# Optimization experiments

Hardware: AMD Instinct MI355X
Metric: run time of the kernel (lower is better)

## Reference

```python
import jax, jax.numpy as jnp
import numpy as np

B, T, S = 32, 32, 400
H, E = 512, 300
V, MAX_OOV = 45000, 50
EXT_V = V + MAX_OOV
NEG = 1.0e12  # INF constant from the torch module


def setup_inputs() -> dict:
    key = jax.random.key(0)
    ks = jax.random.split(key, 16)
    p = lambda k, shape: jax.random.normal(k, shape, jnp.float32) * 0.02
    ext = jax.random.randint(ks[0], (B, S), 0, EXT_V, dtype=jnp.int64 if jax.config.jax_enable_x64 else jnp.int32)
    ext = ext.at[0, 0].set(EXT_V - 1)  # pin max OOV id so num_oov == MAX_OOV (matches torch data-dependent size)
    return {
        "trg_seq_embedded": jax.random.normal(ks[1], (B, T, E), jnp.float32),
        "ext_src_seq": ext,
        "init_states": jax.random.normal(ks[2], (1, B, H), jnp.float32),
        "encoder_outputs": jax.random.normal(ks[3], (B, S, H), jnp.float32),
        "encoder_mask": jnp.ones((B, S), jnp.int32),
        "W_enc": p(ks[4], (H, H)), "b_enc": jnp.zeros((H,), jnp.float32),
        "W_red": p(ks[5], (E, E + H)), "b_red": jnp.zeros((E,), jnp.float32),
        "W_ih": p(ks[6], (4 * H, E)), "W_hh": p(ks[7], (4 * H, H)),
        "b_ih": jnp.zeros((4 * H,), jnp.float32), "b_hh": jnp.zeros((4 * H,), jnp.float32),
        "W_cat": p(ks[8], (H, 2 * H)), "b_cat": jnp.zeros((H,), jnp.float32),
        "W_log": p(ks[9], (V, H)), "b_log": jnp.zeros((V,), jnp.float32),
    }


def reference(trg_seq_embedded, ext_src_seq, init_states, encoder_outputs, encoder_mask,
              W_enc, b_enc, W_red, b_red, W_ih, W_hh, b_ih, b_hh, W_cat, b_cat, W_log, b_log):
    batch = trg_seq_embedded.shape[0]
    # encoder features (memories): [B, S, H]
    memories = jnp.einsum('bsh,gh->bsg', encoder_outputs, W_enc) + b_enc
    batch_idx = jnp.arange(batch)[:, None]
    bias = b_ih + b_hh

    def step(carry, emb):
        h, c, ctx, cov = carry
        # reduce_layer on [embedded ; prev_context] -> [B, E]
        x = jnp.concatenate([emb, ctx], axis=-1) @ W_red.T + b_red
        # single-layer LSTM cell, torch gate order i,f,g,o
        gates = x @ W_ih.T + h @ W_hh.T + bias
        i_g, f_g, g_g, o_g = jnp.split(gates, 4, axis=-1)
        c_new = jax.nn.sigmoid(f_g) * c + jax.nn.sigmoid(i_g) * jnp.tanh(g_g)
        h_new = jax.nn.sigmoid(o_g) * jnp.tanh(c_new)
        # Bahdanau-style dot attention
        energy = jnp.einsum('bh,bsh->bs', h_new, memories)
        energy = jnp.where(encoder_mask == 0, -NEG, energy)
        attn = jax.nn.softmax(energy, axis=1)
        context = jnp.einsum('bs,bsh->bh', attn, memories)
        # output projection
        logit_in = jnp.tanh(jnp.concatenate([h_new, context], axis=-1) @ W_cat.T + b_cat)
        logit = logit_in @ W_log.T + b_log  # [B, V]
        # pointer: scatter_max of energies into extended vocabulary
        ext_logit = jnp.concatenate([logit, jnp.zeros((batch, EXT_V - V), logit.dtype)], axis=1)
        out = jnp.full((batch, EXT_V), -NEG, logit.dtype).at[batch_idx, ext_src_seq].max(energy)
        out = jnp.where(out == -NEG, 0.0, out)
        logit2 = ext_logit + out
        logit2 = jnp.where(logit2 == 0.0, -NEG, logit2)
        return (h_new, c_new, context, cov + attn), (logit2, attn, cov, energy)

    h0 = init_states[0]
    carry0 = (h0, h0, jnp.zeros((batch, memories.shape[-1]), trg_seq_embedded.dtype),
              jnp.zeros((batch, memories.shape[1]), trg_seq_embedded.dtype))
    _, (logits, attn_out, cov_out, energies) = jax.lax.scan(
        step, carry0, jnp.swapaxes(trg_seq_embedded, 0, 1))
    # each stacked over time: logits [T,B,EXT_V], attn/coverage/energies [T,B,S]
    return logits, attn_out, cov_out, energies
```

## Files before the change

### kernel.cpp

```cpp
#include <hip/hip_runtime.h>
#include <hip/hip_bf16.h>

typedef _Float16 h2 __attribute__((ext_vector_type(2)));
typedef _Float16 h8 __attribute__((ext_vector_type(8)));
typedef __attribute__((ext_vector_type(4))) float floatx4;
typedef __attribute__((ext_vector_type(2))) float f32x2;

#define NEGF 1.0e12f

#if __has_builtin(__builtin_amdgcn_fdot2)
#define DOT2(a,b,c) __builtin_amdgcn_fdot2((a),(b),(c),false)
#else
static __device__ __forceinline__ float DOT2(h2 a, h2 b, float c){
  return c + (float)a[0]*(float)b[0] + (float)a[1]*(float)b[1];
}
#endif

__device__ __forceinline__ float dot8(h8 a, h8 b, float c){
  h2 a0 = {a[0],a[1]}, a1 = {a[2],a[3]}, a2 = {a[4],a[5]}, a3 = {a[6],a[7]};
  h2 b0 = {b[0],b[1]}, b1 = {b[2],b[3]}, b2 = {b[4],b[5]}, b3 = {b[6],b[7]};
  c = DOT2(a0,b0,c); c = DOT2(a1,b1,c); c = DOT2(a2,b2,c); c = DOT2(a3,b3,c);
  return c;
}

__device__ __forceinline__ unsigned f16bits(float x){
  union { _Float16 h; unsigned short u; } cv; cv.h = (_Float16)x; return (unsigned)cv.u;
}

#define GLD_LDS16(g, l) __builtin_amdgcn_global_load_lds( \
    (const __attribute__((address_space(1))) void*)(g),   \
    (__attribute__((address_space(3))) void*)(l), 16, 0, 0)

#define ALOAD64(p)    __hip_atomic_load((p), __ATOMIC_RELAXED, __HIP_MEMORY_SCOPE_AGENT)
#define ALOAD32(p)    __hip_atomic_load((p), __ATOMIC_RELAXED, __HIP_MEMORY_SCOPE_AGENT)
#define ASTORE32(p,v) __hip_atomic_store((p), (v), __ATOMIC_RELAXED, __HIP_MEMORY_SCOPE_AGENT)

template<int EPI>
__global__ __launch_bounds__(256) void gemm_f16(
    const _Float16* __restrict__ A, const _Float16* __restrict__ B,
    float* __restrict__ Cf, _Float16* __restrict__ Ch,
    const float* __restrict__ bias, int N, int K, int ldc, int ntn)
{
  __shared__ char smem[32768];
  _Float16* Al = (_Float16*)smem;
  _Float16* Bl = (_Float16*)(smem + 16384);
  int bid = blockIdx.x;
  int bn, bm;
  if (EPI == 3) { bm = bid & 7; bn = bid >> 3; }
  else          { bn = bid % ntn; bm = bid / ntn; }
  int t = threadIdx.x;
  int w = t >> 6, l = t & 63;

  floatx4 acc[4][4];
#pragma unroll
  for (int i = 0; i < 4; ++i)
#pragma unroll
    for (int j = 0; j < 4; ++j) acc[i][j] = (floatx4){0.f, 0.f, 0.f, 0.f};

  const char* Ab = (const char*)A + (size_t)bm * 128 * K * 2;
  const char* Bb = (const char*)B + (size_t)bn * 128 * K * 2;
  const int rowb = K * 2;
  const int r0 = t >> 3;
  const int cbyte = ((t & 7) * 16) ^ (((t >> 3) & 7) << 4);
  char* AlB = (char*)Al;
  char* BlB = (char*)Bl;
  const int wm = (w >> 1) * 64, wn = (w & 1) * 64;

  for (int kt = 0; kt < K; kt += 64) {
    __syncthreads();
#pragma unroll
    for (int c = 0; c < 4; ++c) {
      int row = c * 32 + r0;
      GLD_LDS16(Ab + (size_t)row * rowb + kt * 2 + cbyte, AlB + c * 4096 + t * 16);
      GLD_LDS16(Bb + (size_t)row * rowb + kt * 2 + cbyte, BlB + c * 4096 + t * 16);
    }
    __syncthreads();
#pragma unroll
    for (int kk = 0; kk < 64; kk += 32) {
      h8 af[4], bfv[4];
#pragma unroll
      for (int i = 0; i < 4; ++i) {
        int ra = wm + i * 16 + (l & 15);
        int cb = ((kk << 1) + ((l >> 4) << 4)) ^ ((ra & 7) << 4);
        af[i] = *(const h8*)(AlB + ra * 128 + cb);
      }
#pragma unroll
      for (int j = 0; j < 4; ++j) {
        int ra = wn + j * 16 + (l & 15);
        int cb = ((kk << 1) + ((l >> 4) << 4)) ^ ((ra & 7) << 4);
        bfv[j] = *(const h8*)(BlB + ra * 128 + cb);
      }
#pragma unroll
      for (int i = 0; i < 4; ++i)
#pragma unroll
        for (int j = 0; j < 4; ++j)
          acc[i][j] = __builtin_amdgcn_mfma_f32_16x16x32_f16(af[i], bfv[j], acc[i][j], 0, 0, 0);
    }
  }

  if (EPI == 3) {
    float* Cs = (float*)smem;
#pragma unroll
    for (int half = 0; half < 2; ++half) {
      __syncthreads();
      if ((w >> 1) == half) {
        int rbase = ((l >> 4) << 2);
#pragma unroll
        for (int i = 0; i < 4; ++i)
#pragma unroll
          for (int j = 0; j < 4; ++j)
#pragma unroll
            for (int r = 0; r < 4; ++r)
              Cs[(i * 16 + rbase + r) * 128 + wn + j * 16 + (l & 15)] = acc[i][j][r];
      }
      __syncthreads();
#pragma unroll
      for (int rr = 0; rr < 16; ++rr) {
        int row = rr * 4 + w;
        int grow = bm * 128 + half * 64 + row;
        int cc = bn * 128 + 2 * l;
        float2 v = *(float2*)&Cs[row * 128 + 2 * l];
        float vv0, vv1;
        if (cc < N)     { float x0 = v.x + bias[cc];     vv0 = (x0 == 0.f) ? -NEGF : x0; } else vv0 = -NEGF;
        if (cc + 1 < N) { float x1 = v.y + bias[cc + 1]; vv1 = (x1 == 0.f) ? -NEGF : x1; } else vv1 = -NEGF;
        float* orow = Cf + (size_t)grow * ldc;
        if (cc + 1 < ldc) {
          f32x2 o; o.x = vv0; o.y = vv1;
          __builtin_nontemporal_store(o, (f32x2*)(orow + cc));
        } else if (cc < ldc) {
          __builtin_nontemporal_store(vv0, orow + cc);
        }
      }
    }
  } else {
    int mbase = bm * 128 + wm + ((l >> 4) << 2);
    int nbase = bn * 128 + wn + (l & 15);
#pragma unroll
    for (int j = 0; j < 4; ++j) {
      int col = nbase + j * 16;
#pragma unroll
      for (int i = 0; i < 4; ++i) {
#pragma unroll
        for (int r = 0; r < 4; ++r) {
          int row = mbase + i * 16 + r;
          float v = acc[i][j][r];
          if (col < N) {
            float bv = bias ? bias[col] : 0.f;
            if (EPI == 0)      Cf[(size_t)row * ldc + col] = v + bv;
            else if (EPI == 1) Ch[(size_t)row * ldc + col] = (_Float16)(v + bv);
            else               Ch[(size_t)row * ldc + col] = (_Float16)tanhf(v + bv);
          }
        }
      }
    }
  }
}

__device__ __forceinline__ void castseg(const float* __restrict__ src, _Float16* __restrict__ dst,
                                        int R, int C, int ld_src, int Cpad, int ld_dst, long i){
  int r = (int)(i / Cpad), c = (int)(i % Cpad);
  float v = (r < R && c < C) ? src[(size_t)r * ld_src + c] : 0.f;
  dst[(size_t)r * ld_dst + c] = (_Float16)v;
}

#define SB0 1280
#define SB1 26880
#define SB2 27904
#define SB3 28384
#define SB4 30944
#define SB5 32992
#define SB6 123104
#define SB7 127200
#define SB8 128480
#define SB9 129120

__global__ __launch_bounds__(256) void prep_kernel(
    const float* __restrict__ h0, const float* __restrict__ b_ih, const float* __restrict__ b_hh,
    const float* __restrict__ enc, const float* __restrict__ W_enc, const float* __restrict__ W_red,
    const float* __restrict__ W_ih, const float* __restrict__ W_cat, const float* __restrict__ W_log,
    const float* __restrict__ W_hh, const float* __restrict__ trg,
    _Float16* __restrict__ HCzT, float* __restrict__ bias_sum, _Float16* __restrict__ X1h,
    unsigned* __restrict__ bar, _Float16* __restrict__ enc_h, _Float16* __restrict__ W_enc_h,
    _Float16* __restrict__ Wr1_h, _Float16* __restrict__ W_ih_h, _Float16* __restrict__ W_cat_h,
    _Float16* __restrict__ W_log_h, _Float16* __restrict__ Wz, _Float16* __restrict__ emb_h,
    _Float16* __restrict__ Wr2T_h)
{
  int bid = blockIdx.x, t = threadIdx.x;
  if (bid < SB0) {
    long i = (long)bid * 256 + t;
    if (i < 32768) {
      int unit = (int)(i >> 3), pos = (int)(i & 7);
      int kc = unit >> 5, b = unit & 31;
      int k = kc * 8 + pos;
      HCzT[i] = (k < 512) ? (_Float16)h0[b * 512 + k] : (_Float16)0.f;
    }
    if (i < 2048)  bias_sum[i] = b_ih[i] + b_hh[i];
    if (i < 327680) X1h[i] = (_Float16)0.f;
    if (i < 1024) bar[i] = 0u;
  } else if (bid < SB1) {
    long i = (long)(bid - SB0) * 256 + t;
    castseg(enc, enc_h, 12800, 512, 512, 512, 512, i);
  } else if (bid < SB2) {
    long i = (long)(bid - SB1) * 256 + t;
    castseg(W_enc, W_enc_h, 512, 512, 512, 512, 512, i);
  } else if (bid < SB3) {
    long i = (long)(bid - SB2) * 256 + t;
    castseg(W_red, Wr1_h, 300, 300, 812, 320, 320, i);
  } else if (bid < SB4) {
    long i = (long)(bid - SB3) * 256 + t;
    castseg(W_ih, W_ih_h, 2048, 300, 300, 320, 320, i);
  } else if (bid < SB5) {
    long i = (long)(bid - SB4) * 256 + t;
    castseg(W_cat, W_cat_h, 512, 1024, 1024, 1024, 1024, i);
  } else if (bid < SB6) {
    long i = (long)(bid - SB5) * 256 + t;
    castseg(W_log, W_log_h, 45000, 512, 512, 512, 512, i);
  } else if (bid < SB7) {
    long i = (long)(bid - SB6) * 256 + t;
    castseg(W_hh, Wz, 2048, 512, 512, 512, 1024, i);
  } else if (bid < SB8) {
    int i = (bid - SB7) * 256 + t;
    int m = i / 320, e = i % 320;
    int tt = m >> 5, b = m & 31;
    float v = (e < 300) ? trg[((size_t)b * 32 + tt) * 300 + e] : 0.f;
    emb_h[i] = (_Float16)v;
  } else if (bid < SB9) {
    int i = (bid - SB8) * 256 + t;
    int h = i / 320, e = i % 320;
    float v = (e < 300) ? W_red[(size_t)e * 812 + 300 + h] : 0.f;
    Wr2T_h[i] = (_Float16)v;
  }
}

__device__ __forceinline__ void gbar(unsigned* flags, unsigned gen){
  asm volatile("s_waitcnt vmcnt(0)" ::: "memory");
  __syncthreads();
  if (threadIdx.x == 0) {
    ASTORE32(flags + blockIdx.x, gen);
    for (;;) {
      bool done = true;
#pragma unroll
      for (int i = 0; i < 32; ++i)
        done &= (ALOAD32(flags + i) >= gen);
      if (done) break;
      __builtin_amdgcn_s_sleep(2);
    }
  }
  __syncthreads();
  asm volatile("" ::: "memory");
}

__global__ __launch_bounds__(512, 1) void fused_loop(
    const _Float16* __restrict__ memh, _Float16* __restrict__ HCzT,
    _Float16* __restrict__ HC_A, const _Float16* __restrict__ Wz,
    const float* __restrict__ P, const float* __restrict__ inits,
    const int* __restrict__ mask, float* __restrict__ e_out,
    float* __restrict__ a_out, float* __restrict__ c_out, unsigned* __restrict__ bar)
{
  __shared__ char smem[32768];
  __shared__ __align__(16) float es[400];
  __shared__ float red[16];
  __shared__ float cum[400];
  __shared__ _Float16 hh[512];

  float* gl = (float*)smem;
  const int q = blockIdx.x, t = threadIdx.x;
  const int w = t >> 6, l = t & 63;
  const int mw = w >> 2, nw = w & 3;

  if (t < 400) cum[t] = 0.f;

  float creg = inits[(t >> 4) * 512 + q * 16 + (t & 15)];
  const _Float16* mb = memh + (size_t)q * 400 * 512;

  const _Float16* wbase[4];
#pragma unroll
  for (int s = 0; s < 4; ++s)
    wbase[s] = Wz + (size_t)(s * 512 + q * 16 + (l & 15)) * 1024 + nw * 256 + ((l >> 4) << 3);

  __syncthreads();

  for (int ts = 0; ts < 32; ++ts) {
    {
      unsigned long long* zsrc = (unsigned long long*)(HCzT + (size_t)ts * 32768);
      floatx4 acc[4];
#pragma unroll
      for (int s = 0; s < 4; ++s) acc[s] = (floatx4){0.f, 0.f, 0.f, 0.f};
#pragma unroll
      for (int kk8 = 0; kk8 < 8; ++kk8) {
        int unit = ((nw * 8 + kk8) * 4 + (l >> 4)) * 32 + mw * 16 + (l & 15);
        union { unsigned long long u[2]; h8 v; } za;
        za.u[0] = ALOAD64(zsrc + (size_t)unit * 2);
        za.u[1] = ALOAD64(zsrc + (size_t)unit * 2 + 1);
#pragma unroll
        for (int s = 0; s < 4; ++s) {
          h8 wv = *(const h8*)(wbase[s] + kk8 * 32);
          acc[s] = __builtin_amdgcn_mfma_f32_16x16x32_f16(za.v, wv, acc[s], 0, 0, 0);
        }
      }
#pragma unroll
      for (int s = 0; s < 4; ++s)
#pragma unroll
        for (int r = 0; r < 4; ++r) {
          int b = mw * 16 + ((l >> 4) << 2) + r;
          gl[(s * 4 + nw) * 512 + b * 16 + (l & 15)] = acc[s][r];
        }
    }
    __syncthreads();
    {
      int b = t >> 4, j16 = t & 15;
      const float* Pr = P + ((size_t)ts * 32 + b) * 2048 + q * 16 + j16;
      float g4[4];
#pragma unroll
      for (int s = 0; s < 4; ++s)
        g4[s] = gl[(s * 4 + 0) * 512 + t] + gl[(s * 4 + 1) * 512 + t]
              + gl[(s * 4 + 2) * 512 + t] + gl[(s * 4 + 3) * 512 + t] + Pr[s * 512];
      float ig = 1.f / (1.f + expf(-g4[0]));
      float fg = 1.f / (1.f + expf(-g4[1]));
      float og = 1.f / (1.f + expf(-g4[3]));
      float cn = fg * creg + ig * tanhf(g4[2]);
      float hn = og * tanhf(cn);
      creg = cn;
      unsigned hu = f16bits(hn);
      unsigned other = __shfl_xor(hu, 1);
      if (!(t & 1)) {
        unsigned pack = hu | (other << 16);
        int j = q * 16 + j16;
        unsigned* dst = (unsigned*)((char*)(HCzT + (size_t)(ts + 1) * 32768)
                                    + (((j >> 3) * 32 + b) << 4) + ((j & 7) << 1));
        ASTORE32(dst, pack);
        *(unsigned*)(HC_A + ((size_t)ts * 32 + b) * 1024 + j) = pack;
      }
    }
    gbar(bar, 2 * ts + 1);

    size_t obase = (size_t)ts * 12800 + q * 400;
    {
      if (t < 64) {
        unsigned long long* hsrc = (unsigned long long*)(HCzT + (size_t)(ts + 1) * 32768);
        union { unsigned long long u[2]; h8 v; } ha;
        ha.u[0] = ALOAD64(hsrc + ((size_t)t * 32 + q) * 2);
        ha.u[1] = ALOAD64(hsrc + ((size_t)t * 32 + q) * 2 + 1);
        *(h8*)&hh[t * 8] = ha.v;
      }
      __syncthreads();

      {
        int g = l >> 2, c = l & 3;
#pragma unroll
        for (int r = 0; r < 4; ++r) {
          int sr = r * 16 + g;
          if (sr < 50) {
            int s = w * 50 + sr;
            const _Float16* row = mb + (size_t)s * 512 + c * 128;
            float e = 0.f;
#pragma unroll
            for (int k = 0; k < 16; ++k)
              e = dot8(*(const h8*)(row + k * 8), *(const h8*)&hh[c * 128 + k * 8], e);
            e += __shfl_xor(e, 1);
            e += __shfl_xor(e, 2);
            if (c == 0) {
              if (mask[q * 400 + s] == 0) e = -NEGF;
              es[s] = e;
            }
          }
        }
      }
      __syncthreads();
      if (t < 400) e_out[obase + t] = es[t];

      float v = (t < 400) ? es[t] : -3.4e38f;
      float m = v;
#pragma unroll
      for (int o = 32; o; o >>= 1) m = fmaxf(m, __shfl_xor(m, o));
      if (l == 0) red[w] = m;
      __syncthreads();
      m = red[0];
#pragma unroll
      for (int qq = 1; qq < 8; ++qq) m = fmaxf(m, red[qq]);
      float p = (t < 400) ? expf(v - m) : 0.f;
      float sum = p;
#pragma unroll
      for (int o = 32; o; o >>= 1) sum += __shfl_xor(sum, o);
      if (l == 0) red[8 + w] = sum;
      __syncthreads();
      float tot = red[8];
#pragma unroll
      for (int qq = 9; qq < 16; ++qq) tot += red[qq];
      float inv = 1.f / tot;
      float aval = p * inv;
      if (t < 400) {
        es[t] = aval;
        a_out[obase + t] = aval;
        c_out[obase + t] = cum[t];
        cum[t] += aval;
      }
      __syncthreads();

      float a0 = 0.f, a1 = 0.f, a2 = 0.f, a3 = 0.f;
#pragma unroll 4
      for (int si = 0; si < 400; si += 4) {
        a0 += es[si + 0] * (float)mb[(size_t)(si + 0) * 512 + t];
        a1 += es[si + 1] * (float)mb[(size_t)(si + 1) * 512 + t];
        a2 += es[si + 2] * (float)mb[(size_t)(si + 2) * 512 + t];
        a3 += es[si + 3] * (float)mb[(size_t)(si + 3) * 512 + t];
      }
      float acc2 = (a0 + a1) + (a2 + a3);
      unsigned cu = f16bits(acc2);
      unsigned other = __shfl_xor(cu, 1);
      if (!(t & 1)) {
        unsigned pack = cu | (other << 16);
        int kg = 512 + t;
        unsigned* dst = (unsigned*)((char*)(HCzT + (size_t)(ts + 1) * 32768)
                                    + (((kg >> 3) * 32 + q) << 4) + ((kg & 7) << 1));
        ASTORE32(dst, pack);
        *(unsigned*)(HC_A + ((size_t)ts * 32 + q) * 1024 + kg) = pack;
      }
    }
    gbar(bar, 2 * ts + 2);
  }
}

__global__ __launch_bounds__(512) void pointer_kernel(
    const int* __restrict__ ext, const float* __restrict__ energ, float* __restrict__ logits)
{
  __shared__ int ids[400];
  __shared__ float es[400];
  int tb = blockIdx.x;
  int b = tb & 31;
  int tt = tb >> 5;
  int t = threadIdx.x;
  if (t < 400) {
    ids[t] = ext[b * 400 + t];
    es[t] = energ[(size_t)tt * 12800 + b * 400 + t];
  }
  __syncthreads();
  if (t < 400) {
    int id = ids[t];
    bool first = true;
    for (int s = 0; s < t; ++s) if (ids[s] == id) { first = false; break; }
    if (first) {
      float mx = es[t];
      for (int s = t + 1; s < 400; ++s) if (ids[s] == id) mx = fmaxf(mx, es[s]);
      if (mx != -NEGF) {
        float* p = &logits[(size_t)tb * 45050 + id];
        float base = 0.f;
        if (id < 45000) { float cur = *p; base = (cur == -NEGF) ? 0.f : cur; }
        float nv = base + mx;
        *p = (nv == 0.f) ? -NEGF : nv;
      }
    }
  }
}

extern "C" void kernel_launch(void* const* d_in, const int* in_sizes, int n_in,
                              void* d_out, int out_size, void* d_ws, size_t ws_size,
                              hipStream_t stream) {
  const float* trg   = (const float*)d_in[0];
  const int*   ext   = (const int*)d_in[1];
  const float* inits = (const float*)d_in[2];
  const float* enc   = (const float*)d_in[3];
  const int*   mask  = (const int*)d_in[4];
  const float* W_enc = (const float*)d_in[5];
  const float* b_enc = (const float*)d_in[6];
  const float* W_red = (const float*)d_in[7];
  const float* b_red = (const float*)d_in[8];
  const float* W_ih  = (const float*)d_in[9];
  const float* W_hh  = (const float*)d_in[10];
  const float* b_ih  = (const float*)d_in[11];
  const float* b_hh  = (const float*)d_in[12];
  const float* W_cat = (const float*)d_in[13];
  const float* b_cat = (const float*)d_in[14];
  const float* W_log = (const float*)d_in[15];
  const float* b_log = (const float*)d_in[16];

  float* out = (float*)d_out;
  float* out_logits = out;
  float* out_attn   = out + 46131200;
  float* out_cov    = out_attn + 409600;
  float* out_energy = out_cov + 409600;

  char* ws = (char*)d_ws;
  size_t o = 0;
  auto alloc = [&](size_t bytes) { void* p = ws + o; o += (bytes + 255) & ~(size_t)255; return p; };
  _Float16* mem_h   = (_Float16*)alloc(12800ULL * 512 * 2);
  _Float16* enc_h   = (_Float16*)alloc(12800ULL * 512 * 2);
  _Float16* W_enc_h = (_Float16*)alloc(512ULL * 512 * 2);
  _Float16* emb_h   = (_Float16*)alloc(1024ULL * 320 * 2);
  _Float16* Wr1_h   = (_Float16*)alloc(384ULL * 320 * 2);
  _Float16* X1_h    = (_Float16*)alloc(1024ULL * 320 * 2);
  _Float16* W_ih_h  = (_Float16*)alloc(2048ULL * 320 * 2);
  _Float16* Wr2T_h  = (_Float16*)alloc(512ULL * 320 * 2);
  _Float16* W_cat_h = (_Float16*)alloc(512ULL * 1024 * 2);
  _Float16* W_log_h = (_Float16*)alloc(45056ULL * 512 * 2);
  _Float16* A_log_h = (_Float16*)alloc(1024ULL * 512 * 2);
  _Float16* HCzT    = (_Float16*)alloc(33ULL * 32768 * 2);
  _Float16* HC_A    = (_Float16*)alloc(1024ULL * 1024 * 2);
  _Float16* Wz      = (_Float16*)alloc(2048ULL * 1024 * 2);
  float* P        = (float*)alloc(1024ULL * 2048 * 4);
  float* bias_sum = (float*)alloc(2048ULL * 4);
  unsigned* bar   = (unsigned*)alloc(4096);

  prep_kernel<<<SB9, 256, 0, stream>>>(
      inits, b_ih, b_hh, enc, W_enc, W_red, W_ih, W_cat, W_log, W_hh, trg,
      HCzT, bias_sum, X1_h, bar, enc_h, W_enc_h, Wr1_h, W_ih_h, W_cat_h,
      W_log_h, Wz, emb_h, Wr2T_h);

  gemm_f16<1><<<400, 256, 0, stream>>>(enc_h, W_enc_h, nullptr, mem_h, b_enc, 512, 512, 512, 4);
  gemm_f16<1><<<24,  256, 0, stream>>>(emb_h, Wr1_h, nullptr, X1_h, b_red, 300, 320, 320, 3);
  gemm_f16<0><<<128, 256, 0, stream>>>(X1_h, W_ih_h, P, nullptr, bias_sum, 2048, 320, 2048, 16);
  gemm_f16<1><<<64,  256, 0, stream>>>(W_ih_h, Wr2T_h, nullptr, Wz + 512, nullptr, 512, 320, 1024, 4);

  fused_loop<<<32, 512, 0, stream>>>(mem_h, HCzT, HC_A, Wz, P, inits, mask,
                                     out_energy, out_attn, out_cov, bar);

  gemm_f16<2><<<32, 256, 0, stream>>>(HC_A, W_cat_h, nullptr, A_log_h, b_cat, 512, 1024, 512, 4);
  gemm_f16<3><<<2816, 256, 0, stream>>>(A_log_h, W_log_h, out_logits, nullptr, b_log, 45000, 512, 45050, 352);
  pointer_kernel<<<1024, 512, 0, stream>>>(ext, out_energy, out_logits);
}
```

Before: 1.186 ms.

## Overlap vocab projection GEMMs with the recurrent loop inside one persistent kernel

Merges the recurrent loop, the W_cat projection and the vocabulary logits GEMM into a single persistent kernel of 256 blocks. The first 32 blocks run the timestep recurrence and publish a progress counter. The other 224 blocks wait on that counter, then compute the tanh(W_cat) and W_log GEMMs for each completed chunk of 4 timesteps while later steps are still running. The aim is to hide the large logits GEMM behind the latency-bound recurrence. In exchange it adds spin-wait synchronisation, assumes all 256 blocks are co-resident, and drops the separate GEMM launches.

```diff
diff --git a/kernel.cpp b/kernel.cpp
--- a/kernel.cpp
+++ b/kernel.cpp
@@ -45,9 +45,7 @@
   _Float16* Al = (_Float16*)smem;
   _Float16* Bl = (_Float16*)(smem + 16384);
   int bid = blockIdx.x;
-  int bn, bm;
-  if (EPI == 3) { bm = bid & 7; bn = bid >> 3; }
-  else          { bn = bid % ntn; bm = bid / ntn; }
+  int bn = bid % ntn, bm = bid / ntn;
   int t = threadIdx.x;
   int w = t >> 6, l = t & 63;
 
@@ -98,58 +96,126 @@
     }
   }
 
-  if (EPI == 3) {
-    float* Cs = (float*)smem;
-#pragma unroll
-    for (int half = 0; half < 2; ++half) {
-      __syncthreads();
-      if ((w >> 1) == half) {
-        int rbase = ((l >> 4) << 2);
+  int mbase = bm * 128 + wm + ((l >> 4) << 2);
+  int nbase = bn * 128 + wn + (l & 15);
+#pragma unroll
+  for (int j = 0; j < 4; ++j) {
+    int col = nbase + j * 16;
+#pragma unroll
+    for (int i = 0; i < 4; ++i) {
+#pragma unroll
+      for (int r = 0; r < 4; ++r) {
+        int row = mbase + i * 16 + r;
+        float v = acc[i][j][r];
+        if (col < N) {
+          float bv = bias ? bias[col] : 0.f;
+          if (EPI == 0) Cf[(size_t)row * ldc + col] = v + bv;
+          else          Ch[(size_t)row * ldc + col] = (_Float16)(v + bv);
+        }
+      }
+    }
+  }
+}
+
+template<int EPI>
+__device__ void wgemm(const _Float16* __restrict__ Aext, int lda,
+                      const _Float16* __restrict__ B,
+                      float* __restrict__ Cf, _Float16* __restrict__ Alog,
+                      const float* __restrict__ bias,
+                      int N, int K, int ldc, int bm, int bn, char* smem)
+{
+  int t = threadIdx.x;
+  bool act = t < 256;
+  int w = t >> 6, l = t & 63;
+  floatx4 acc[4][4];
+#pragma unroll
+  for (int i = 0; i < 4; ++i)
+#pragma unroll
+    for (int j = 0; j < 4; ++j) acc[i][j] = (floatx4){0.f, 0.f, 0.f, 0.f};
+
+  const char* Bb = (const char*)B + (size_t)bn * 128 * K * 2;
+  const int rowb = K * 2;
+  const int r0 = t >> 3;
+  const int cbyte = ((t & 7) * 16) ^ (((t >> 3) & 7) << 4);
+  char* BlB = smem;
+  const int wm = (w >> 1) * 64, wn = (w & 1) * 64;
+
+  for (int kt = 0; kt < K; kt += 64) {
+    __syncthreads();
+    if (act) {
+#pragma unroll
+      for (int c = 0; c < 4; ++c) {
+        int row = c * 32 + r0;
+        GLD_LDS16(Bb + (size_t)row * rowb + kt * 2 + cbyte, BlB + c * 4096 + t * 16);
+      }
+    }
+    __syncthreads();
+    if (act) {
+#pragma unroll
+      for (int kk = 0; kk < 64; kk += 32) {
+        h8 af[4], bfv[4];
+#pragma unroll
+        for (int i = 0; i < 4; ++i) {
+          int ra = wm + i * 16 + (l & 15);
+          unsigned long long* ap = (unsigned long long*)
+              (Aext + (size_t)ra * lda + kt + kk + ((l >> 4) << 3));
+          union { unsigned long long u[2]; h8 v; } ua;
+          ua.u[0] = ALOAD64(ap); ua.u[1] = ALOAD64(ap + 1);
+          af[i] = ua.v;
+        }
+#pragma unroll
+        for (int j = 0; j < 4; ++j) {
+          int ra = wn + j * 16 + (l & 15);
+          int cb = ((kk << 1) + ((l >> 4) << 4)) ^ ((ra & 7) << 4);
+          bfv[j] = *(const h8*)(BlB + ra * 128 + cb);
+        }
 #pragma unroll
         for (int i = 0; i < 4; ++i)
 #pragma unroll
           for (int j = 0; j < 4; ++j)
-#pragma unroll
-            for (int r = 0; r < 4; ++r)
-              Cs[(i * 16 + rbase + r) * 128 + wn + j * 16 + (l & 15)] = acc[i][j][r];
-      }
-      __syncthreads();
+            acc[i][j] = __builtin_amdgcn_mfma_f32_16x16x32_f16(af[i], bfv[j], acc[i][j], 0, 0, 0);
+      }
+    }
+  }
+
+  float* Cs = (float*)smem;
+#pragma unroll
+  for (int half = 0; half < 2; ++half) {
+    __syncthreads();
+    if (act && (w >> 1) == half) {
+      int rbase = ((l >> 4) << 2);
+#pragma unroll
+      for (int i = 0; i < 4; ++i)
+#pragma unroll
+        for (int j = 0; j < 4; ++j)
+#pragma unroll
+          for (int r = 0; r < 4; ++r)
+            Cs[(i * 16 + rbase + r) * 128 + wn + j * 16 + (l & 15)] = acc[i][j][r];
+    }
+    __syncthreads();
+    if (act) {
 #pragma unroll
       for (int rr = 0; rr < 16; ++rr) {
         int row = rr * 4 + w;
         int grow = bm * 128 + half * 64 + row;
         int cc = bn * 128 + 2 * l;
         float2 v = *(float2*)&Cs[row * 128 + 2 * l];
-        float vv0, vv1;
-        if (cc < N)     { float x0 = v.x + bias[cc];     vv0 = (x0 == 0.f) ? -NEGF : x0; } else vv0 = -NEGF;
-        if (cc + 1 < N) { float x1 = v.y + bias[cc + 1]; vv1 = (x1 == 0.f) ? -NEGF : x1; } else vv1 = -NEGF;
-        float* orow = Cf + (size_t)grow * ldc;
-        if (cc + 1 < ldc) {
-          f32x2 o; o.x = vv0; o.y = vv1;
-          __builtin_nontemporal_store(o, (f32x2*)(orow + cc));
-        } else if (cc < ldc) {
-          __builtin_nontemporal_store(vv0, orow + cc);
-        }
-      }
-    }
-  } else {
-    int mbase = bm * 128 + wm + ((l >> 4) << 2);
-    int nbase = bn * 128 + wn + (l & 15);
-#pragma unroll
-    for (int j = 0; j < 4; ++j) {
-      int col = nbase + j * 16;
-#pragma unroll
-      for (int i = 0; i < 4; ++i) {
-#pragma unroll
-        for (int r = 0; r < 4; ++r) {
-          int row = mbase + i * 16 + r;
-          float v = acc[i][j][r];
-          if (col < N) {
-            float bv = bias ? bias[col] : 0.f;
-            if (EPI == 0)      Cf[(size_t)row * ldc + col] = v + bv;
-            else if (EPI == 1) Ch[(size_t)row * ldc + col] = (_Float16)(v + bv);
-            else               Ch[(size_t)row * ldc + col] = (_Float16)tanhf(v + bv);
+        if (EPI == 3) {
+          float vv0, vv1;
+          if (cc < N)     { float x0 = v.x + bias[cc];     vv0 = (x0 == 0.f) ? -NEGF : x0; } else vv0 = -NEGF;
+          if (cc + 1 < N) { float x1 = v.y + bias[cc + 1]; vv1 = (x1 == 0.f) ? -NEGF : x1; } else vv1 = -NEGF;
+          float* orow = Cf + (size_t)grow * ldc;
+          if (cc + 1 < ldc) {
+            f32x2 o; o.x = vv0; o.y = vv1;
+            __builtin_nontemporal_store(o, (f32x2*)(orow + cc));
+          } else if (cc < ldc) {
+            __builtin_nontemporal_store(vv0, orow + cc);
           }
+        } else {
+          float x0 = tanhf(v.x + bias[cc]);
+          float x1 = tanhf(v.y + bias[cc + 1]);
+          unsigned pack = f16bits(x0) | (f16bits(x1) << 16);
+          ASTORE32((unsigned*)(Alog + (size_t)grow * 512 + cc), pack);
         }
       }
     }
@@ -250,12 +316,15 @@
   asm volatile("" ::: "memory");
 }
 
-__global__ __launch_bounds__(512, 1) void fused_loop(
+__global__ __launch_bounds__(512, 1) void fused_all(
     const _Float16* __restrict__ memh, _Float16* __restrict__ HCzT,
     _Float16* __restrict__ HC_A, const _Float16* __restrict__ Wz,
     const float* __restrict__ P, const float* __restrict__ inits,
     const int* __restrict__ mask, float* __restrict__ e_out,
-    float* __restrict__ a_out, float* __restrict__ c_out, unsigned* __restrict__ bar)
+    float* __restrict__ a_out, float* __restrict__ c_out, unsigned* __restrict__ bar,
+    const _Float16* __restrict__ W_cat_h, const float* __restrict__ b_cat,
+    _Float16* __restrict__ A_log, const _Float16* __restrict__ W_log_h,
+    const float* __restrict__ b_log, float* __restrict__ logits)
 {
   __shared__ char smem[32768];
   __shared__ __align__(16) float es[400];
@@ -263,161 +332,193 @@
   __shared__ float cum[400];
   __shared__ _Float16 hh[512];
 
-  float* gl = (float*)smem;
-  const int q = blockIdx.x, t = threadIdx.x;
-  const int w = t >> 6, l = t & 63;
-  const int mw = w >> 2, nw = w & 3;
-
-  if (t < 400) cum[t] = 0.f;
-
-  float creg = inits[(t >> 4) * 512 + q * 16 + (t & 15)];
-  const _Float16* mb = memh + (size_t)q * 400 * 512;
-
-  const _Float16* wbase[4];
-#pragma unroll
-  for (int s = 0; s < 4; ++s)
-    wbase[s] = Wz + (size_t)(s * 512 + q * 16 + (l & 15)) * 1024 + nw * 256 + ((l >> 4) << 3);
-
-  __syncthreads();
-
-  for (int ts = 0; ts < 32; ++ts) {
-    {
-      unsigned long long* zsrc = (unsigned long long*)(HCzT + (size_t)ts * 32768);
-      floatx4 acc[4];
-#pragma unroll
-      for (int s = 0; s < 4; ++s) acc[s] = (floatx4){0.f, 0.f, 0.f, 0.f};
-#pragma unroll
-      for (int kk8 = 0; kk8 < 8; ++kk8) {
-        int unit = ((nw * 8 + kk8) * 4 + (l >> 4)) * 32 + mw * 16 + (l & 15);
-        union { unsigned long long u[2]; h8 v; } za;
-        za.u[0] = ALOAD64(zsrc + (size_t)unit * 2);
-        za.u[1] = ALOAD64(zsrc + (size_t)unit * 2 + 1);
-#pragma unroll
-        for (int s = 0; s < 4; ++s) {
-          h8 wv = *(const h8*)(wbase[s] + kk8 * 32);
-          acc[s] = __builtin_amdgcn_mfma_f32_16x16x32_f16(za.v, wv, acc[s], 0, 0, 0);
-        }
-      }
-#pragma unroll
-      for (int s = 0; s < 4; ++s)
-#pragma unroll
-        for (int r = 0; r < 4; ++r) {
-          int b = mw * 16 + ((l >> 4) << 2) + r;
-          gl[(s * 4 + nw) * 512 + b * 16 + (l & 15)] = acc[s][r];
-        }
-    }
+  const int blk = blockIdx.x, t = threadIdx.x;
+
+  if (blk < 32) {
+    float* gl = (float*)smem;
+    const int q = blk;
+    const int w = t >> 6, l = t & 63;
+    const int mw = w >> 2, nw = w & 3;
+
+    if (t < 400) cum[t] = 0.f;
+
+    float creg = inits[(t >> 4) * 512 + q * 16 + (t & 15)];
+    const _Float16* mb = memh + (size_t)q * 400 * 512;
+
+    const _Float16* wbase[4];
+#pragma unroll
+    for (int s = 0; s < 4; ++s)
+      wbase[s] = Wz + (size_t)(s * 512 + q * 16 + (l & 15)) * 1024 + nw * 256 + ((l >> 4) << 3);
+
     __syncthreads();
-    {
-      int b = t >> 4, j16 = t & 15;
-      const float* Pr = P + ((size_t)ts * 32 + b) * 2048 + q * 16 + j16;
-      float g4[4];
-#pragma unroll
-      for (int s = 0; s < 4; ++s)
-        g4[s] = gl[(s * 4 + 0) * 512 + t] + gl[(s * 4 + 1) * 512 + t]
-              + gl[(s * 4 + 2) * 512 + t] + gl[(s * 4 + 3) * 512 + t] + Pr[s * 512];
-      float ig = 1.f / (1.f + expf(-g4[0]));
-      float fg = 1.f / (1.f + expf(-g4[1]));
-      float og = 1.f / (1.f + expf(-g4[3]));
-      float cn = fg * creg + ig * tanhf(g4[2]);
-      float hn = og * tanhf(cn);
-      creg = cn;
-      unsigned hu = f16bits(hn);
-      unsigned other = __shfl_xor(hu, 1);
-      if (!(t & 1)) {
-        unsigned pack = hu | (other << 16);
-        int j = q * 16 + j16;
-        unsigned* dst = (unsigned*)((char*)(HCzT + (size_t)(ts + 1) * 32768)
-                                    + (((j >> 3) * 32 + b) << 4) + ((j & 7) << 1));
-        ASTORE32(dst, pack);
-        *(unsigned*)(HC_A + ((size_t)ts * 32 + b) * 1024 + j) = pack;
-      }
-    }
-    gbar(bar, 2 * ts + 1);
-
-    size_t obase = (size_t)ts * 12800 + q * 400;
-    {
-      if (t < 64) {
-        unsigned long long* hsrc = (unsigned long long*)(HCzT + (size_t)(ts + 1) * 32768);
-        union { unsigned long long u[2]; h8 v; } ha;
-        ha.u[0] = ALOAD64(hsrc + ((size_t)t * 32 + q) * 2);
-        ha.u[1] = ALOAD64(hsrc + ((size_t)t * 32 + q) * 2 + 1);
-        *(h8*)&hh[t * 8] = ha.v;
+
+    for (int ts = 0; ts < 32; ++ts) {
+      {
+        unsigned long long* zsrc = (unsigned long long*)(HCzT + (size_t)ts * 32768);
+        floatx4 acc[4];
+#pragma unroll
+        for (int s = 0; s < 4; ++s) acc[s] = (floatx4){0.f, 0.f, 0.f, 0.f};
+#pragma unroll
+        for (int kk8 = 0; kk8 < 8; ++kk8) {
+          int unit = ((nw * 8 + kk8) * 4 + (l >> 4)) * 32 + mw * 16 + (l & 15);
+          union { unsigned long long u[2]; h8 v; } za;
+          za.u[0] = ALOAD64(zsrc + (size_t)unit * 2);
+          za.u[1] = ALOAD64(zsrc + (size_t)unit * 2 + 1);
+#pragma unroll
+          for (int s = 0; s < 4; ++s) {
+            h8 wv = *(const h8*)(wbase[s] + kk8 * 32);
+            acc[s] = __builtin_amdgcn_mfma_f32_16x16x32_f16(za.v, wv, acc[s], 0, 0, 0);
+          }
+        }
+#pragma unroll
+        for (int s = 0; s < 4; ++s)
+#pragma unroll
+          for (int r = 0; r < 4; ++r) {
+            int b = mw * 16 + ((l >> 4) << 2) + r;
+            gl[(s * 4 + nw) * 512 + b * 16 + (l & 15)] = acc[s][r];
+          }
       }
       __syncthreads();
-
       {
-        int g = l >> 2, c = l & 3;
-#pragma unroll
-        for (int r = 0; r < 4; ++r) {
-          int sr = r * 16 + g;
-          if (sr < 50) {
-            int s = w * 50 + sr;
-            const _Float16* row = mb + (size_t)s * 512 + c * 128;
-            float e = 0.f;
-#pragma unroll
-            for (int k = 0; k < 16; ++k)
-              e = dot8(*(const h8*)(row + k * 8), *(const h8*)&hh[c * 128 + k * 8], e);
-            e += __shfl_xor(e, 1);
-            e += __shfl_xor(e, 2);
-            if (c == 0) {
-              if (mask[q * 400 + s] == 0) e = -NEGF;
-              es[s] = e;
+        int b = t >> 4, j16 = t & 15;
+        const float* Pr = P + ((size_t)ts * 32 + b) * 2048 + q * 16 + j16;
+        float g4[4];
+#pragma unroll
+        for (int s = 0; s < 4; ++s)
+          g4[s] = gl[(s * 4 + 0) * 512 + t] + gl[(s * 4 + 1) * 512 + t]
+                + gl[(s * 4 + 2) * 512 + t] + gl[(s * 4 + 3) * 512 + t] + Pr[s * 512];
+        float ig = 1.f / (1.f + expf(-g4[0]));
+        float fg = 1.f / (1.f + expf(-g4[1]));
+        float og = 1.f / (1.f + expf(-g4[3]));
+        float cn = fg * creg + ig * tanhf(g4[2]);
+        float hn = og * tanhf(cn);
+        creg = cn;
+        unsigned hu = f16bits(hn);
+        unsigned other = __shfl_xor(hu, 1);
+        if (!(t & 1)) {
+          unsigned pack = hu | (other << 16);
+          int j = q * 16 + j16;
+          unsigned* dst = (unsigned*)((char*)(HCzT + (size_t)(ts + 1) * 32768)
+                                      + (((j >> 3) * 32 + b) << 4) + ((j & 7) << 1));
+          ASTORE32(dst, pack);
+          ASTORE32((unsigned*)(HC_A + ((size_t)ts * 32 + b) * 1024 + j), pack);
+        }
+      }
+      gbar(bar, 2 * ts + 1);
+
+      size_t obase = (size_t)ts * 12800 + q * 400;
+      {
+        if (t < 64) {
+          unsigned long long* hsrc = (unsigned long long*)(HCzT + (size_t)(ts + 1) * 32768);
+          union { unsigned long long u[2]; h8 v; } ha;
+          ha.u[0] = ALOAD64(hsrc + ((size_t)t * 32 + q) * 2);
+          ha.u[1] = ALOAD64(hsrc + ((size_t)t * 32 + q) * 2 + 1);
+          *(h8*)&hh[t * 8] = ha.v;
+        }
+        __syncthreads();
+
+        {
+          int g = l >> 2, c = l & 3;
+#pragma unroll
+          for (int r = 0; r < 4; ++r) {
+            int sr = r * 16 + g;
+            if (sr < 50) {
+              int s = w * 50 + sr;
+              const _Float16* row = mb + (size_t)s * 512 + c * 128;
+              float e = 0.f;
+#pragma unroll
+              for (int k = 0; k < 16; ++k)
+                e = dot8(*(const h8*)(row + k * 8), *(const h8*)&hh[c * 128 + k * 8], e);
+              e += __shfl_xor(e, 1);
+              e += __shfl_xor(e, 2);
+              if (c == 0) {
+                if (mask[q * 400 + s] == 0) e = -NEGF;
+                es[s] = e;
+              }
             }
           }
         }
+        __syncthreads();
+        if (t < 400) e_out[obase + t] = es[t];
+
+        float v = (t < 400) ? es[t] : -3.4e38f;
+        float m = v;
+#pragma unroll
+        for (int o = 32; o; o >>= 1) m = fmaxf(m, __shfl_xor(m, o));
+        if (l == 0) red[w] = m;
+        __syncthreads();
+        m = red[0];
+#pragma unroll
+        for (int qq = 1; qq < 8; ++qq) m = fmaxf(m, red[qq]);
+        float p = (t < 400) ? expf(v - m) : 0.f;
+        float sum = p;
+#pragma unroll
+        for (int o = 32; o; o >>= 1) sum += __shfl_xor(sum, o);
+        if (l == 0) red[8 + w] = sum;
+        __syncthreads();
+        float tot = red[8];
+#pragma unroll
+        for (int qq = 9; qq < 16; ++qq) tot += red[qq];
+        float inv = 1.f / tot;
+        float aval = p * inv;
+        if (t < 400) {
+          es[t] = aval;
+          a_out[obase + t] = aval;
+          c_out[obase + t] = cum[t];
+          cum[t] += aval;
+        }
+        __syncthreads();
+
+        float a0 = 0.f, a1 = 0.f, a2 = 0.f, a3 = 0.f;
+#pragma unroll 4
+        for (int si = 0; si < 400; si += 4) {
+          a0 += es[si + 0] * (float)mb[(size_t)(si + 0) * 512 + t];
+          a1 += es[si + 1] * (float)mb[(size_t)(si + 1) * 512 + t];
+          a2 += es[si + 2] * (float)mb[(size_t)(si + 2) * 512 + t];
+          a3 += es[si + 3] * (float)mb[(size_t)(si + 3) * 512 + t];
+        }
+        float acc2 = (a0 + a1) + (a2 + a3);
+        unsigned cu = f16bits(acc2);
+        unsigned other = __shfl_xor(cu, 1);
+        if (!(t & 1)) {
+          unsigned pack = cu | (other << 16);
+          int kg = 512 + t;
+          unsigned* dst = (unsigned*)((char*)(HCzT + (size_t)(ts + 1) * 32768)
+                                      + (((kg >> 3) * 32 + q) << 4) + ((kg & 7) << 1));
+          ASTORE32(dst, pack);
+          ASTORE32((unsigned*)(HC_A + ((size_t)ts * 32 + q) * 1024 + kg), pack);
+        }
+      }
+      gbar(bar, 2 * ts + 2);
+      if (blk == 0 && t == 0) ASTORE32(bar + 256, (unsigned)(ts + 1));
+    }
+  } else {
+    int wid = blk - 32;
+    unsigned* prog = bar + 256;
+    unsigned* cnt  = bar + 512;
+    for (int c = 0; c < 8; ++c) {
+      if (t == 0) {
+        while (ALOAD32(prog) < (unsigned)(4 * c + 4)) __builtin_amdgcn_s_sleep(8);
       }
       __syncthreads();
-      if (t < 400) e_out[obase + t] = es[t];
-
-      float v = (t < 400) ? es[t] : -3.4e38f;
-      float m = v;
-#pragma unroll
-      for (int o = 32; o; o >>= 1) m = fmaxf(m, __shfl_xor(m, o));
-      if (l == 0) red[w] = m;
+      if (wid >= c * 4 && wid < c * 4 + 4) {
+        wgemm<2>(HC_A + (size_t)c * 128 * 1024, 1024, W_cat_h, nullptr, A_log, b_cat,
+                 512, 1024, 512, c, wid - c * 4, smem);
+        asm volatile("s_waitcnt vmcnt(0)" ::: "memory");
+        __syncthreads();
+        if (t == 0)
+          __hip_atomic_fetch_add(cnt + c, 1u, __ATOMIC_RELAXED, __HIP_MEMORY_SCOPE_AGENT);
+      }
+      if (t == 0) {
+        while (ALOAD32(cnt + c) < 4u) __builtin_amdgcn_s_sleep(2);
+      }
       __syncthreads();
-      m = red[0];
-#pragma unroll
-      for (int qq = 1; qq < 8; ++qq) m = fmaxf(m, red[qq]);
-      float p = (t < 400) ? expf(v - m) : 0.f;
-      float sum = p;
-#pragma unroll
-      for (int o = 32; o; o >>= 1) sum += __shfl_xor(sum, o);
-      if (l == 0) red[8 + w] = sum;
-      __syncthreads();
-      float tot = red[8];
-#pragma unroll
-      for (int qq = 9; qq < 16; ++qq) tot += red[qq];
-      float inv = 1.f / tot;
-      float aval = p * inv;
-      if (t < 400) {
-        es[t] = aval;
-        a_out[obase + t] = aval;
-        c_out[obase + t] = cum[t];
-        cum[t] += aval;
-      }
-      __syncthreads();
-
-      float a0 = 0.f, a1 = 0.f, a2 = 0.f, a3 = 0.f;
-#pragma unroll 4
-      for (int si = 0; si < 400; si += 4) {
-        a0 += es[si + 0] * (float)mb[(size_t)(si + 0) * 512 + t];
-        a1 += es[si + 1] * (float)mb[(size_t)(si + 1) * 512 + t];
-        a2 += es[si + 2] * (float)mb[(size_t)(si + 2) * 512 + t];
-        a3 += es[si + 3] * (float)mb[(size_t)(si + 3) * 512 + t];
-      }
-      float acc2 = (a0 + a1) + (a2 + a3);
-      unsigned cu = f16bits(acc2);
-      unsigned other = __shfl_xor(cu, 1);
-      if (!(t & 1)) {
-        unsigned pack = cu | (other << 16);
-        int kg = 512 + t;
-        unsigned* dst = (unsigned*)((char*)(HCzT + (size_t)(ts + 1) * 32768)
-                                    + (((kg >> 3) * 32 + q) << 4) + ((kg & 7) << 1));
-        ASTORE32(dst, pack);
-        *(unsigned*)(HC_A + ((size_t)ts * 32 + q) * 1024 + kg) = pack;
-      }
-    }
-    gbar(bar, 2 * ts + 2);
+      wgemm<3>(A_log + (size_t)c * 128 * 512, 512, W_log_h, logits, nullptr, b_log,
+               45000, 512, 45050, c, wid, smem);
+      if (wid + 224 < 352)
+        wgemm<3>(A_log + (size_t)c * 128 * 512, 512, W_log_h, logits, nullptr, b_log,
+                 45000, 512, 45050, c, wid + 224, smem);
+    }
   }
 }
 
@@ -511,10 +612,9 @@
   gemm_f16<0><<<128, 256, 0, stream>>>(X1_h, W_ih_h, P, nullptr, bias_sum, 2048, 320, 2048, 16);
   gemm_f16<1><<<64,  256, 0, stream>>>(W_ih_h, Wr2T_h, nullptr, Wz + 512, nullptr, 512, 320, 1024, 4);
 
-  fused_loop<<<32, 512, 0, stream>>>(mem_h, HCzT, HC_A, Wz, P, inits, mask,
-                                     out_energy, out_attn, out_cov, bar);
-
-  gemm_f16<2><<<32, 256, 0, stream>>>(HC_A, W_cat_h, nullptr, A_log_h, b_cat, 512, 1024, 512, 4);
-  gemm_f16<3><<<2816, 256, 0, stream>>>(A_log_h, W_log_h, out_logits, nullptr, b_log, 45000, 512, 45050, 352);
+  fused_all<<<256, 512, 0, stream>>>(mem_h, HCzT, HC_A, Wz, P, inits, mask,
+                                     out_energy, out_attn, out_cov, bar,
+                                     W_cat_h, b_cat, A_log_h, W_log_h, b_log, out_logits);
+
   pointer_kernel<<<1024, 512, 0, stream>>>(ext, out_energy, out_logits);
 }
```

New measurement: 1.222 ms. 3.0% more time.
